# Optimization experiments

Hardware: AMD Instinct MI355X
Metric: run time of the kernel (lower is better)

Reference implementation:

```python
import jax, jax.numpy as jnp
import numpy as np

NA = 3        # anchors per scale
NC = 80       # classes
NO = NC + 5   # outputs per anchor
STRIDES = (8.0, 16.0, 32.0)


def setup_inputs() -> dict:
    key = jax.random.key(0)
    ks = jax.random.split(key, 10)
    inp = {
        "p0": jax.random.normal(ks[0], (16, 256, 80, 80), jnp.float32),
        "p1": jax.random.normal(ks[1], (16, 512, 40, 40), jnp.float32),
        "p2": jax.random.normal(ks[2], (16, 1024, 20, 20), jnp.float32),
        "w0": jax.random.normal(ks[3], (255, 256), jnp.float32) * 0.02,
        "b0": jax.random.normal(ks[4], (255,), jnp.float32) * 0.02,
        "w1": jax.random.normal(ks[5], (255, 512), jnp.float32) * 0.02,
        "b1": jax.random.normal(ks[6], (255,), jnp.float32) * 0.02,
        "w2": jax.random.normal(ks[7], (255, 1024), jnp.float32) * 0.02,
        "b2": jax.random.normal(ks[8], (255,), jnp.float32) * 0.02,
        # YOLOv5 default anchors (pixel units), shape [nl, na, 2]
        "anchors": jnp.asarray(np.array(
            [[[10, 13], [16, 30], [33, 23]],
             [[30, 61], [62, 45], [59, 119]],
             [[116, 90], [156, 198], [373, 326]]], dtype=np.float32)),
    }
    return inp


def _decode_scale(p, w, b, anc, stride):
    # p: [bs, C, ny, nx]; w: [na*no, C]; anc: [na, 2] pixel anchors
    bs, _, ny, nx = p.shape
    y = jnp.einsum('bchw,oc->bohw', p, w) + b[None, :, None, None]   # 1x1 conv
    y = y.reshape(bs, NA, NO, ny, nx).transpose(0, 1, 3, 4, 2)       # [bs,na,ny,nx,no]
    s = jax.nn.sigmoid(y)
    gy, gx = jnp.meshgrid(jnp.arange(ny, dtype=p.dtype),
                          jnp.arange(nx, dtype=p.dtype), indexing='ij')
    grid = jnp.stack((gx, gy), axis=-1)[None, None] - 0.5            # [1,1,ny,nx,2]
    xy = (s[..., :2] * 2 + grid) * stride
    wh = (s[..., 2:4] * 2) ** 2 * anc.reshape(1, NA, 1, 1, 2)
    out = jnp.concatenate((xy, wh, s[..., 4:]), axis=-1)
    return out.reshape(bs, NA * ny * nx, NO)


def reference(p0, p1, p2, w0, b0, w1, b1, w2, b2, anchors):
    feats = (p0, p1, p2)
    ws = (w0, w1, w2)
    bs_ = (b0, b1, b2)
    z = [_decode_scale(feats[i], ws[i], bs_[i], anchors[i], STRIDES[i])
         for i in range(3)]
    return jnp.concatenate(z, axis=1)  # [bs, sum(na*ny*nx), no]
```

## Files before the change

kernel.cpp:

```cpp
#include <hip/hip_runtime.h>
#include <math.h>


#define NOUT 85
#define TOTAL_ROWS 25200

typedef __attribute__((ext_vector_type(8))) short short8;
typedef __attribute__((ext_vector_type(4))) float floatx4;

__device__ __forceinline__ unsigned short f2bf(float x) {
    union { float f; unsigned u; } v; v.f = x;
    unsigned r = v.u + 0x7fffu + ((v.u >> 16) & 1u);
    return (unsigned short)(r >> 16);
}

__global__ __launch_bounds__(256) void convert_w_all(
    const float* __restrict__ w0, const float* __restrict__ w1,
    const float* __restrict__ w2, unsigned short* __restrict__ dst)
{
    int i = blockIdx.x * 256 + threadIdx.x;
    const float* w; int C, idx;
    if (i < 65536)       { w = w0; C = 256;  idx = i; }
    else if (i < 196608) { w = w1; C = 512;  idx = i - 65536; }
    else                 { w = w2; C = 1024; idx = i - 196608; }
    int j  = idx & 7;
    int l  = (idx >> 3) & 63;
    int t  = idx >> 9;
    int ot = t & 15, kt = t >> 4;
    int o  = ot * 16 + (l & 15);
    int k  = kt * 32 + (l >> 4) * 8 + j;
    float v = (o < 255) ? w[(size_t)o * C + k] : 0.f;
    dst[i] = f2bf(v);
}

__global__ __launch_bounds__(256) void yolo_fused(
    const float* __restrict__ p0, const float* __restrict__ p1,
    const float* __restrict__ p2, const unsigned short* __restrict__ wsA,
    const float* __restrict__ b0v, const float* __restrict__ b1v,
    const float* __restrict__ b2v, const float* __restrict__ anc,
    float* __restrict__ out)
{
    __shared__ __align__(16) unsigned short Bl0[64 * 32];
    __shared__ __align__(16) unsigned short Bl1[64 * 32];

    const int tid = threadIdx.x;
    const int l   = tid & 63;
    const int wv  = tid >> 6;
    const int ml  = l & 15;
    const int q   = l >> 4;

    const int x = blockIdx.x;
    const float* p; const unsigned short* wA; const float* bias; const float* an;
    int C, HW, row_off, sh, tile, b; float stride_;
    if (x < 112) {
        b = x / 7;  tile = x - b * 7;
        p = p2; wA = wsA + 196608; bias = b2v; an = anc + 12;
        C = 1024; HW = 400; row_off = 24000; sh = 2; stride_ = 32.f;
    } else if (x < 512) {
        int i = x - 112; b = i / 25; tile = i - b * 25;
        p = p1; wA = wsA + 65536; bias = b1v; an = anc + 6;
        C = 512; HW = 1600; row_off = 19200; sh = 3; stride_ = 16.f;
    } else {
        int i = x - 512; b = i / 100; tile = i - b * 100;
        p = p0; wA = wsA; bias = b0v; an = anc;
        C = 256; HW = 6400; row_off = 0; sh = 4; stride_ = 8.f;
    }
    const int hw0   = tile * 64;
    const int iters = C >> 5;

    floatx4 acc[4][4];
#pragma unroll
    for (int ni = 0; ni < 4; ++ni)
#pragma unroll
        for (int mi = 0; mi < 4; ++mi)
            acc[ni][mi] = floatx4{0.f, 0.f, 0.f, 0.f};

    const float* pb = p + (size_t)b * C * HW;
    int scol = hw0 + l; if (scol >= HW) scol = HW - 1;
    const float* pcol0 = pb + (size_t)(wv * 8) * HW + scol;
    const size_t kj = (size_t)32 * HW;

    const int wchunk = wv ^ (l & 3) ^ ((l >> 2) & 3);
    const unsigned short* wfb = wA + ((size_t)(wv * 4) << 9) + (l << 3);

    float  bvA[8], bvB[8];
    short8 wfA[4], wfB[4];

#define LOADBV(dst, s) do { const float* _pc = pcol0 + (size_t)(s) * kj;          \
        _Pragma("unroll") for (int _r = 0; _r < 8; ++_r)                          \
            dst[_r] = _pc[(size_t)_r * HW]; } while (0)
#define LOADWF(dst, s) do { const unsigned short* _wb = wfb + (size_t)(s) * 8192; \
        _Pragma("unroll") for (int _m = 0; _m < 4; ++_m)                          \
            dst[_m] = *(const short8*)(_wb + (_m << 9)); } while (0)
#define PACK(src, BUF) do {                                                       \
        unsigned _p0 = (unsigned)f2bf(src[0]) | ((unsigned)f2bf(src[1]) << 16);   \
        unsigned _p1 = (unsigned)f2bf(src[2]) | ((unsigned)f2bf(src[3]) << 16);   \
        unsigned _p2 = (unsigned)f2bf(src[4]) | ((unsigned)f2bf(src[5]) << 16);   \
        unsigned _p3 = (unsigned)f2bf(src[6]) | ((unsigned)f2bf(src[7]) << 16);   \
        ((uint4*)BUF)[l * 4 + wchunk] = make_uint4(_p0, _p1, _p2, _p3); } while (0)
#define READPF(pf, BUF) do { _Pragma("unroll") for (int _n = 0; _n < 4; ++_n) {   \
        int _nn = _n * 16 + ml; int _ck = q ^ (_nn & 3) ^ ((_nn >> 2) & 3);       \
        pf[_n] = *(const short8*)(BUF + _nn * 32 + _ck * 8); } } while (0)
#define MFMA16(pf, wf) do { _Pragma("unroll") for (int _n = 0; _n < 4; ++_n)      \
        _Pragma("unroll") for (int _m = 0; _m < 4; ++_m)                          \
            acc[_n][_m] = __builtin_amdgcn_mfma_f32_16x16x32_bf16(                \
                pf[_n], wf[_m], acc[_n][_m], 0, 0, 0); } while (0)
#define LGKM_BARRIER() do { asm volatile("s_waitcnt lgkmcnt(0)" ::: "memory");    \
        __builtin_amdgcn_s_barrier(); asm volatile("" ::: "memory"); } while (0)

    LOADBV(bvA, 0);
    LOADBV(bvB, 1);
    LOADWF(wfA, 0);
    PACK(bvA, Bl0);
    LOADBV(bvA, 2);
    LGKM_BARRIER();

    for (int it = 0; it < iters; it += 2) {
        short8 pfA[4];
        READPF(pfA, Bl0);
        PACK(bvB, Bl1);
        if (it + 3 < iters) LOADBV(bvB, it + 3);
        LOADWF(wfB, it + 1);
        LGKM_BARRIER();
        MFMA16(pfA, wfA);

        short8 pfB[4];
        READPF(pfB, Bl1);
        if (it + 2 < iters) {
            PACK(bvA, Bl0);
            if (it + 4 < iters) LOADBV(bvA, it + 4);
            LOADWF(wfA, it + 2);
            LGKM_BARRIER();
        }
        MFMA16(pfB, wfB);
    }

    const int nx = 5 << sh;
#pragma unroll
    for (int mi = 0; mi < 4; ++mi) {
        const int  o     = wv * 64 + mi * 16 + ml;
        const bool valid = (o < 255);
        const int  osafe = valid ? o : 254;
        const int  a     = osafe / 85;
        const int  oo    = osafe - a * 85;
        const float bi   = bias[osafe];
        const float anw  = an[a * 2 + 0];
        const float anh  = an[a * 2 + 1];
        float* orow = out + ((size_t)b * TOTAL_ROWS + row_off + a * HW) * NOUT + oo;
#pragma unroll
        for (int ni = 0; ni < 4; ++ni) {
            const int hwb = hw0 + ni * 16 + q * 4;
            if (hwb >= HW) continue;
#pragma unroll
            for (int r = 0; r < 4; ++r) {
                const int hw = hwb + r;
                float y = acc[ni][mi][r] + bi;
                float s = 1.f / (1.f + __expf(-y));
                float v;
                if (oo >= 4) {
                    v = s;
                } else {
                    unsigned gy = (unsigned)(((unsigned long long)(unsigned)(hw >> sh)
                                             * 0xCCCCCCCDull) >> 34);
                    int gx = hw - (int)gy * nx;
                    if (oo == 0)      v = (2.f * s + (float)gx - 0.5f) * stride_;
                    else if (oo == 1) v = (2.f * s + (float)gy - 0.5f) * stride_;
                    else { float t = 2.f * s; v = t * t * ((oo == 2) ? anw : anh); }
                }
                if (valid) orow[(size_t)hw * NOUT] = v;
            }
        }
    }
#undef LOADBV
#undef LOADWF
#undef PACK
#undef READPF
#undef MFMA16
#undef LGKM_BARRIER
}

extern "C" void kernel_launch(void* const* d_in, const int* in_sizes, int n_in,
                              void* d_out, int out_size, void* d_ws, size_t ws_size,
                              hipStream_t stream) {
    const float* p0 = (const float*)d_in[0];
    const float* p1 = (const float*)d_in[1];
    const float* p2 = (const float*)d_in[2];
    const float* w0 = (const float*)d_in[3];
    const float* b0 = (const float*)d_in[4];
    const float* w1 = (const float*)d_in[5];
    const float* b1 = (const float*)d_in[6];
    const float* w2 = (const float*)d_in[7];
    const float* b2 = (const float*)d_in[8];
    const float* anc = (const float*)d_in[9];
    float* out = (float*)d_out;

    unsigned short* wsA = (unsigned short*)d_ws;

    convert_w_all<<<dim3(458752 / 256), dim3(256), 0, stream>>>(w0, w1, w2, wsA);

    yolo_fused<<<dim3(2112), dim3(256), 0, stream>>>(
        p0, p1, p2, wsA, b0, b1, b2, anc, out);
}
```

Measured before the change: 339.9 us.

## Pre-convert activations to bf16 MFMA fragment layout in separate pass

Adds a pre-pass kernel that converts all three feature maps to bf16 and writes them to workspace in the exact MFMA fragment order. A new GEMM kernel then loads activation and weight fragments straight from global memory into registers, with no LDS staging and no barriers, double-buffering the loads. This removes the per-block packing and synchronisation, at the cost of an extra full read of the fp32 inputs plus a bf16 write and re-read. The new path runs only when the workspace is large enough, and otherwise falls back to the fused kernel.

New measurement: 374.7 us. 1.1x slower.

```diff
diff --git a/kernel.cpp b/kernel.cpp
--- a/kernel.cpp
+++ b/kernel.cpp
@@ -4,6 +4,18 @@
 
 #define NOUT 85
 #define TOTAL_ROWS 25200
+
+#define WOFF0 0
+#define WOFF1 65536
+#define WOFF2 196608
+#define PFRAG_OFF 458752
+#define PSZ0 26214400
+#define PSZ1 13107200
+#define PSZ2 7340032
+#define POFF0 (PFRAG_OFF)
+#define POFF1 (PFRAG_OFF + PSZ0)
+#define POFF2 (PFRAG_OFF + PSZ0 + PSZ1)
+#define WS_NEED_FULL ((size_t)(PFRAG_OFF + PSZ0 + PSZ1 + PSZ2) * 2)
 
 typedef __attribute__((ext_vector_type(8))) short short8;
 typedef __attribute__((ext_vector_type(4))) float floatx4;
@@ -33,6 +45,147 @@
     dst[i] = f2bf(v);
 }
 
+__global__ __launch_bounds__(256) void convert_p_all(
+    const float* __restrict__ p0, const float* __restrict__ p1,
+    const float* __restrict__ p2, unsigned short* __restrict__ ws)
+{
+    int i = blockIdx.x * 256 + threadIdx.x;
+    const float* p; int C, HW; int b, t, s, lc;
+    if (i < 3276800) {
+        p = p0; C = 256; HW = 6400;
+        lc = i & 255; s = (i >> 8) & 7;  int bt = i >> 11;
+        b = bt / 100; t = bt - b * 100;
+    } else if (i < 4915200) {
+        int idx = i - 3276800;
+        p = p1; C = 512; HW = 1600;
+        lc = idx & 255; s = (idx >> 8) & 15; int bt = idx >> 12;
+        b = bt / 25;  t = bt - b * 25;
+    } else {
+        int idx = i - 4915200;
+        p = p2; C = 1024; HW = 400;
+        lc = idx & 255; s = (idx >> 8) & 31; int bt = idx >> 13;
+        b = bt / 7;   t = bt - b * 7;
+    }
+    int ni = lc >> 6, l = lc & 63, q = l >> 4, ml = l & 15;
+    int hw = t * 64 + ni * 16 + ml; if (hw >= HW) hw = HW - 1;
+    const float* src = p + ((size_t)b * C + (s * 32 + q * 8)) * HW + hw;
+    unsigned d[4];
+#pragma unroll
+    for (int r = 0; r < 4; ++r) {
+        float a  = src[(size_t)(2 * r) * HW];
+        float bb = src[(size_t)(2 * r + 1) * HW];
+        d[r] = (unsigned)f2bf(a) | ((unsigned)f2bf(bb) << 16);
+    }
+    ((uint4*)(ws + PFRAG_OFF))[(size_t)i] = make_uint4(d[0], d[1], d[2], d[3]);
+}
+
+__global__ __launch_bounds__(256) void yolo_gemm(
+    const unsigned short* __restrict__ ws,
+    const float* __restrict__ b0v, const float* __restrict__ b1v,
+    const float* __restrict__ b2v, const float* __restrict__ anc,
+    float* __restrict__ out)
+{
+    const int tid = threadIdx.x;
+    const int l   = tid & 63;
+    const int wv  = tid >> 6;
+    const int ml  = l & 15;
+    const int q   = l >> 4;
+
+    const int x = blockIdx.x;
+    const float* bias; const float* an;
+    int C, HW, row_off, sh, tile, b, T; size_t wOff, pOff; float stride_;
+    if (x < 112) {
+        b = x / 7;  tile = x - b * 7;  T = 7;
+        wOff = WOFF2; pOff = POFF2; bias = b2v; an = anc + 12;
+        C = 1024; HW = 400; row_off = 24000; sh = 2; stride_ = 32.f;
+    } else if (x < 512) {
+        int i = x - 112; b = i / 25; tile = i - b * 25; T = 25;
+        wOff = WOFF1; pOff = POFF1; bias = b1v; an = anc + 6;
+        C = 512; HW = 1600; row_off = 19200; sh = 3; stride_ = 16.f;
+    } else {
+        int i = x - 512; b = i / 100; tile = i - b * 100; T = 100;
+        wOff = WOFF0; pOff = POFF0; bias = b0v; an = anc;
+        C = 256; HW = 6400; row_off = 0; sh = 4; stride_ = 8.f;
+    }
+    const int hw0 = tile * 64;
+    const int S   = C >> 5;
+
+    const unsigned short* pfp = ws + pOff + (size_t)(b * T + tile) * S * 2048 + (l << 3);
+    const unsigned short* wfp = ws + wOff + ((size_t)(wv * 4) << 9) + (l << 3);
+
+    floatx4 acc[4][4];
+#pragma unroll
+    for (int ni = 0; ni < 4; ++ni)
+#pragma unroll
+        for (int mi = 0; mi < 4; ++mi)
+            acc[ni][mi] = floatx4{0.f, 0.f, 0.f, 0.f};
+
+#define GLOADP(dst, s_) do { const unsigned short* _b = pfp + (size_t)(s_) * 2048;  \
+        _Pragma("unroll") for (int _n = 0; _n < 4; ++_n)                            \
+            dst[_n] = *(const short8*)(_b + (_n << 9)); } while (0)
+#define GLOADW(dst, s_) do { const unsigned short* _b = wfp + (size_t)(s_) * 8192;  \
+        _Pragma("unroll") for (int _m = 0; _m < 4; ++_m)                            \
+            dst[_m] = *(const short8*)(_b + (_m << 9)); } while (0)
+#define GMFMA(pf, wf) do { _Pragma("unroll") for (int _n = 0; _n < 4; ++_n)         \
+        _Pragma("unroll") for (int _m = 0; _m < 4; ++_m)                            \
+            acc[_n][_m] = __builtin_amdgcn_mfma_f32_16x16x32_bf16(                  \
+                pf[_n], wf[_m], acc[_n][_m], 0, 0, 0); } while (0)
+
+    short8 pfA[4], wfA[4], pfB[4], wfB[4];
+    GLOADP(pfA, 0); GLOADW(wfA, 0);
+    GLOADP(pfB, 1); GLOADW(wfB, 1);
+
+    int s = 0;
+    for (; s + 2 < S; s += 2) {
+        GMFMA(pfA, wfA);
+        GLOADP(pfA, s + 2); GLOADW(wfA, s + 2);
+        GMFMA(pfB, wfB);
+        GLOADP(pfB, s + 3); GLOADW(wfB, s + 3);
+    }
+    GMFMA(pfA, wfA);
+    GMFMA(pfB, wfB);
+#undef GLOADP
+#undef GLOADW
+#undef GMFMA
+
+    const int nx = 5 << sh;
+#pragma unroll
+    for (int mi = 0; mi < 4; ++mi) {
+        const int  o     = wv * 64 + mi * 16 + ml;
+        const bool valid = (o < 255);
+        const int  osafe = valid ? o : 254;
+        const int  a     = osafe / 85;
+        const int  oo    = osafe - a * 85;
+        const float bi   = bias[osafe];
+        const float anw  = an[a * 2 + 0];
+        const float anh  = an[a * 2 + 1];
+        float* orow = out + ((size_t)b * TOTAL_ROWS + row_off + a * HW) * NOUT + oo;
+#pragma unroll
+        for (int ni = 0; ni < 4; ++ni) {
+            const int hwb = hw0 + ni * 16 + q * 4;
+            if (hwb >= HW) continue;
+#pragma unroll
+            for (int r = 0; r < 4; ++r) {
+                const int hw = hwb + r;
+                float y = acc[ni][mi][r] + bi;
+                float sg = 1.f / (1.f + __expf(-y));
+                float v;
+                if (oo >= 4) {
+                    v = sg;
+                } else {
+                    unsigned gy = (unsigned)(((unsigned long long)(unsigned)(hw >> sh)
+                                             * 0xCCCCCCCDull) >> 34);
+                    int gx = hw - (int)gy * nx;
+                    if (oo == 0)      v = (2.f * sg + (float)gx - 0.5f) * stride_;
+                    else if (oo == 1) v = (2.f * sg + (float)gy - 0.5f) * stride_;
+                    else { float tt = 2.f * sg; v = tt * tt * ((oo == 2) ? anw : anh); }
+                }
+                if (valid) orow[(size_t)hw * NOUT] = v;
+            }
+        }
+    }
+}
+
 __global__ __launch_bounds__(256) void yolo_fused(
     const float* __restrict__ p0, const float* __restrict__ p1,
     const float* __restrict__ p2, const unsigned short* __restrict__ wsA,
@@ -54,15 +207,15 @@
     int C, HW, row_off, sh, tile, b; float stride_;
     if (x < 112) {
         b = x / 7;  tile = x - b * 7;
-        p = p2; wA = wsA + 196608; bias = b2v; an = anc + 12;
+        p = p2; wA = wsA + WOFF2; bias = b2v; an = anc + 12;
         C = 1024; HW = 400; row_off = 24000; sh = 2; stride_ = 32.f;
     } else if (x < 512) {
         int i = x - 112; b = i / 25; tile = i - b * 25;
-        p = p1; wA = wsA + 65536; bias = b1v; an = anc + 6;
+        p = p1; wA = wsA + WOFF1; bias = b1v; an = anc + 6;
         C = 512; HW = 1600; row_off = 19200; sh = 3; stride_ = 16.f;
     } else {
         int i = x - 512; b = i / 100; tile = i - b * 100;
-        p = p0; wA = wsA; bias = b0v; an = anc;
+        p = p0; wA = wsA + WOFF0; bias = b0v; an = anc;
         C = 256; HW = 6400; row_off = 0; sh = 4; stride_ = 8.f;
     }
     const int hw0   = tile * 64;
@@ -155,17 +308,17 @@
             for (int r = 0; r < 4; ++r) {
                 const int hw = hwb + r;
                 float y = acc[ni][mi][r] + bi;
-                float s = 1.f / (1.f + __expf(-y));
+                float sg = 1.f / (1.f + __expf(-y));
                 float v;
                 if (oo >= 4) {
-                    v = s;
+                    v = sg;
                 } else {
                     unsigned gy = (unsigned)(((unsigned long long)(unsigned)(hw >> sh)
                                              * 0xCCCCCCCDull) >> 34);
                     int gx = hw - (int)gy * nx;
-                    if (oo == 0)      v = (2.f * s + (float)gx - 0.5f) * stride_;
-                    else if (oo == 1) v = (2.f * s + (float)gy - 0.5f) * stride_;
-                    else { float t = 2.f * s; v = t * t * ((oo == 2) ? anw : anh); }
+                    if (oo == 0)      v = (2.f * sg + (float)gx - 0.5f) * stride_;
+                    else if (oo == 1) v = (2.f * sg + (float)gy - 0.5f) * stride_;
+                    else { float tt = 2.f * sg; v = tt * tt * ((oo == 2) ? anw : anh); }
                 }
                 if (valid) orow[(size_t)hw * NOUT] = v;
             }
@@ -198,6 +351,12 @@
 
     convert_w_all<<<dim3(458752 / 256), dim3(256), 0, stream>>>(w0, w1, w2, wsA);
 
-    yolo_fused<<<dim3(2112), dim3(256), 0, stream>>>(
-        p0, p1, p2, wsA, b0, b1, b2, anc, out);
-}
+    if (ws_size >= WS_NEED_FULL) {
+        convert_p_all<<<dim3(22784), dim3(256), 0, stream>>>(p0, p1, p2, wsA);
+        yolo_gemm<<<dim3(2112), dim3(256), 0, stream>>>(
+            wsA, b0, b1, b2, anc, out);
+    } else {
+        yolo_fused<<<dim3(2112), dim3(256), 0, stream>>>(
+            p0, p1, p2, wsA, b0, b1, b2, anc, out);
+    }
+}
```

## Stage activation chunks in shared memory and coalesce output via LDS staging

Applied to the files above, without the earlier changes.

Replaces the per-iteration double-buffered activation pipeline with bulk chunked loads: each chunk of up to 512 channels is read as float4 vectors, converted to bf16 and stored into a swizzled 64KB shared buffer, then the MFMA loop runs over it. The epilogue writes results into shared memory and then copies them to global memory contiguously, instead of doing scattered stores with an 85-float stride. This targets uncoalesced loads and stores, but the 64KB LDS lowers occupancy and drops the overlap of loads with compute inside each chunk.

New measurement: 330.7 us. 2.7% less time.

```diff
diff --git a/kernel.cpp b/kernel.cpp
--- a/kernel.cpp
+++ b/kernel.cpp
@@ -4,6 +4,10 @@
 
 #define NOUT 85
 #define TOTAL_ROWS 25200
+
+#define WOFF0 0
+#define WOFF1 65536
+#define WOFF2 196608
 
 typedef __attribute__((ext_vector_type(8))) short short8;
 typedef __attribute__((ext_vector_type(4))) float floatx4;
@@ -33,15 +37,16 @@
     dst[i] = f2bf(v);
 }
 
-__global__ __launch_bounds__(256) void yolo_fused(
+__global__ __launch_bounds__(256) void yolo_fused2(
     const float* __restrict__ p0, const float* __restrict__ p1,
     const float* __restrict__ p2, const unsigned short* __restrict__ wsA,
     const float* __restrict__ b0v, const float* __restrict__ b1v,
     const float* __restrict__ b2v, const float* __restrict__ anc,
     float* __restrict__ out)
 {
-    __shared__ __align__(16) unsigned short Bl0[64 * 32];
-    __shared__ __align__(16) unsigned short Bl1[64 * 32];
+    __shared__ __align__(16) unsigned char smem[65536];
+    unsigned short* act = (unsigned short*)smem;
+    float*          ob  = (float*)smem;
 
     const int tid = threadIdx.x;
     const int l   = tid & 63;
@@ -54,19 +59,21 @@
     int C, HW, row_off, sh, tile, b; float stride_;
     if (x < 112) {
         b = x / 7;  tile = x - b * 7;
-        p = p2; wA = wsA + 196608; bias = b2v; an = anc + 12;
+        p = p2; wA = wsA + WOFF2; bias = b2v; an = anc + 12;
         C = 1024; HW = 400; row_off = 24000; sh = 2; stride_ = 32.f;
     } else if (x < 512) {
         int i = x - 112; b = i / 25; tile = i - b * 25;
-        p = p1; wA = wsA + 65536; bias = b1v; an = anc + 6;
+        p = p1; wA = wsA + WOFF1; bias = b1v; an = anc + 6;
         C = 512; HW = 1600; row_off = 19200; sh = 3; stride_ = 16.f;
     } else {
         int i = x - 512; b = i / 100; tile = i - b * 100;
-        p = p0; wA = wsA; bias = b0v; an = anc;
+        p = p0; wA = wsA + WOFF0; bias = b0v; an = anc;
         C = 256; HW = 6400; row_off = 0; sh = 4; stride_ = 8.f;
     }
-    const int hw0   = tile * 64;
-    const int iters = C >> 5;
+    const int hw0 = tile * 64;
+    const int S   = C >> 5;
+    const int Sc  = (S < 16) ? S : 16;
+    const int nch = (S > 16) ? (S >> 4) : 1;
 
     floatx4 acc[4][4];
 #pragma unroll
@@ -75,66 +82,71 @@
         for (int mi = 0; mi < 4; ++mi)
             acc[ni][mi] = floatx4{0.f, 0.f, 0.f, 0.f};
 
+    const int s_loc = tid >> 6;
+    const int co    = (tid >> 4) & 3;
+    const int hq    = tid & 15;
+    int hwq = hw0 + hq * 4;
+    if (hwq + 4 > HW) hwq = HW - 4;
     const float* pb = p + (size_t)b * C * HW;
-    int scol = hw0 + l; if (scol >= HW) scol = HW - 1;
-    const float* pcol0 = pb + (size_t)(wv * 8) * HW + scol;
-    const size_t kj = (size_t)32 * HW;
-
-    const int wchunk = wv ^ (l & 3) ^ ((l >> 2) & 3);
-    const unsigned short* wfb = wA + ((size_t)(wv * 4) << 9) + (l << 3);
-
-    float  bvA[8], bvB[8];
-    short8 wfA[4], wfB[4];
-
-#define LOADBV(dst, s) do { const float* _pc = pcol0 + (size_t)(s) * kj;          \
-        _Pragma("unroll") for (int _r = 0; _r < 8; ++_r)                          \
-            dst[_r] = _pc[(size_t)_r * HW]; } while (0)
-#define LOADWF(dst, s) do { const unsigned short* _wb = wfb + (size_t)(s) * 8192; \
-        _Pragma("unroll") for (int _m = 0; _m < 4; ++_m)                          \
-            dst[_m] = *(const short8*)(_wb + (_m << 9)); } while (0)
-#define PACK(src, BUF) do {                                                       \
-        unsigned _p0 = (unsigned)f2bf(src[0]) | ((unsigned)f2bf(src[1]) << 16);   \
-        unsigned _p1 = (unsigned)f2bf(src[2]) | ((unsigned)f2bf(src[3]) << 16);   \
-        unsigned _p2 = (unsigned)f2bf(src[4]) | ((unsigned)f2bf(src[5]) << 16);   \
-        unsigned _p3 = (unsigned)f2bf(src[6]) | ((unsigned)f2bf(src[7]) << 16);   \
-        ((uint4*)BUF)[l * 4 + wchunk] = make_uint4(_p0, _p1, _p2, _p3); } while (0)
-#define READPF(pf, BUF) do { _Pragma("unroll") for (int _n = 0; _n < 4; ++_n) {   \
-        int _nn = _n * 16 + ml; int _ck = q ^ (_nn & 3) ^ ((_nn >> 2) & 3);       \
-        pf[_n] = *(const short8*)(BUF + _nn * 32 + _ck * 8); } } while (0)
-#define MFMA16(pf, wf) do { _Pragma("unroll") for (int _n = 0; _n < 4; ++_n)      \
-        _Pragma("unroll") for (int _m = 0; _m < 4; ++_m)                          \
-            acc[_n][_m] = __builtin_amdgcn_mfma_f32_16x16x32_bf16(                \
+
+    const unsigned short* wfp = wA + ((size_t)(wv * 4) << 9) + (l << 3);
+
+#define LOADWF(dst, s_) do { const unsigned short* _b = wfp + (size_t)(s_) * 8192;  \
+        _Pragma("unroll") for (int _m = 0; _m < 4; ++_m)                            \
+            dst[_m] = *(const short8*)(_b + (_m << 9)); } while (0)
+#define READPF(pf, s_) do { _Pragma("unroll") for (int _n = 0; _n < 4; ++_n) {      \
+        int _a16 = (((s_) * 4 + _n) << 6) + l; _a16 ^= (_a16 >> 4) & 7;             \
+        pf[_n] = *(const short8*)(act + (_a16 << 3)); } } while (0)
+#define GMFMA(pf, wf) do { _Pragma("unroll") for (int _n = 0; _n < 4; ++_n)         \
+        _Pragma("unroll") for (int _m = 0; _m < 4; ++_m)                            \
+            acc[_n][_m] = __builtin_amdgcn_mfma_f32_16x16x32_bf16(                  \
                 pf[_n], wf[_m], acc[_n][_m], 0, 0, 0); } while (0)
-#define LGKM_BARRIER() do { asm volatile("s_waitcnt lgkmcnt(0)" ::: "memory");    \
-        __builtin_amdgcn_s_barrier(); asm volatile("" ::: "memory"); } while (0)
-
-    LOADBV(bvA, 0);
-    LOADBV(bvB, 1);
-    LOADWF(wfA, 0);
-    PACK(bvA, Bl0);
-    LOADBV(bvA, 2);
-    LGKM_BARRIER();
-
-    for (int it = 0; it < iters; it += 2) {
-        short8 pfA[4];
-        READPF(pfA, Bl0);
-        PACK(bvB, Bl1);
-        if (it + 3 < iters) LOADBV(bvB, it + 3);
-        LOADWF(wfB, it + 1);
-        LGKM_BARRIER();
-        MFMA16(pfA, wfA);
-
-        short8 pfB[4];
-        READPF(pfB, Bl1);
-        if (it + 2 < iters) {
-            PACK(bvA, Bl0);
-            if (it + 4 < iters) LOADBV(bvA, it + 4);
-            LOADWF(wfA, it + 2);
-            LGKM_BARRIER();
+
+    for (int ch = 0; ch < nch; ++ch) {
+        if (ch) __syncthreads();
+        const int cb = ch * Sc * 32;
+
+        for (int r = 0; r < (Sc >> 2); ++r) {
+            const int s = r * 4 + s_loc;
+            const int c = cb + s * 32 + co * 8;
+            floatx4 v[8];
+#pragma unroll
+            for (int i = 0; i < 8; ++i)
+                v[i] = *(const floatx4*)(pb + (size_t)(c + i) * HW + hwq);
+#pragma unroll
+            for (int e = 0; e < 4; ++e) {
+                const int hwr = hq * 4 + e;
+                const int ni = hwr >> 4, mll = hwr & 15;
+                unsigned d0 = (unsigned)f2bf(v[0][e]) | ((unsigned)f2bf(v[1][e]) << 16);
+                unsigned d1 = (unsigned)f2bf(v[2][e]) | ((unsigned)f2bf(v[3][e]) << 16);
+                unsigned d2 = (unsigned)f2bf(v[4][e]) | ((unsigned)f2bf(v[5][e]) << 16);
+                unsigned d3 = (unsigned)f2bf(v[6][e]) | ((unsigned)f2bf(v[7][e]) << 16);
+                int a16 = ((s * 4 + ni) << 6) + co * 16 + mll;
+                a16 ^= (a16 >> 4) & 7;
+                *(uint4*)(act + (a16 << 3)) = make_uint4(d0, d1, d2, d3);
+            }
         }
-        MFMA16(pfB, wfB);
-    }
-
+        __syncthreads();
+
+        const int gs0 = ch * Sc;
+        short8 wfA[4], wfB[4];
+        LOADWF(wfA, gs0);
+        LOADWF(wfB, gs0 + 1);
+        for (int s = 0; s < Sc; s += 2) {
+            short8 pfA[4], pfB[4];
+            READPF(pfA, s);
+            GMFMA(pfA, wfA);
+            if (s + 2 < Sc) LOADWF(wfA, gs0 + s + 2);
+            READPF(pfB, s + 1);
+            GMFMA(pfB, wfB);
+            if (s + 3 < Sc) LOADWF(wfB, gs0 + s + 3);
+        }
+    }
+#undef LOADWF
+#undef READPF
+#undef GMFMA
+
+    __syncthreads();
     const int nx = 5 << sh;
 #pragma unroll
     for (int mi = 0; mi < 4; ++mi) {
@@ -146,37 +158,44 @@
         const float bi   = bias[osafe];
         const float anw  = an[a * 2 + 0];
         const float anh  = an[a * 2 + 1];
-        float* orow = out + ((size_t)b * TOTAL_ROWS + row_off + a * HW) * NOUT + oo;
+        const int  lbase = a * 5440 + oo;
 #pragma unroll
         for (int ni = 0; ni < 4; ++ni) {
-            const int hwb = hw0 + ni * 16 + q * 4;
-            if (hwb >= HW) continue;
-#pragma unroll
-            for (int r = 0; r < 4; ++r) {
-                const int hw = hwb + r;
-                float y = acc[ni][mi][r] + bi;
-                float s = 1.f / (1.f + __expf(-y));
+            const int hwr0 = ni * 16 + q * 4;
+            if (hw0 + hwr0 >= HW) continue;
+#pragma unroll
+            for (int rr = 0; rr < 4; ++rr) {
+                const int hwr = hwr0 + rr;
+                const int hw  = hw0 + hwr;
+                float y  = acc[ni][mi][rr] + bi;
+                float sg = 1.f / (1.f + __expf(-y));
                 float v;
                 if (oo >= 4) {
-                    v = s;
+                    v = sg;
                 } else {
                     unsigned gy = (unsigned)(((unsigned long long)(unsigned)(hw >> sh)
                                              * 0xCCCCCCCDull) >> 34);
                     int gx = hw - (int)gy * nx;
-                    if (oo == 0)      v = (2.f * s + (float)gx - 0.5f) * stride_;
-                    else if (oo == 1) v = (2.f * s + (float)gy - 0.5f) * stride_;
-                    else { float t = 2.f * s; v = t * t * ((oo == 2) ? anw : anh); }
+                    if (oo == 0)      v = (2.f * sg + (float)gx - 0.5f) * stride_;
+                    else if (oo == 1) v = (2.f * sg + (float)gy - 0.5f) * stride_;
+                    else { float tt = 2.f * sg; v = tt * tt * ((oo == 2) ? anw : anh); }
                 }
-                if (valid) orow[(size_t)hw * NOUT] = v;
+                if (valid) ob[lbase + hwr * 85] = v;
             }
         }
     }
-#undef LOADBV
-#undef LOADWF
-#undef PACK
-#undef READPF
-#undef MFMA16
-#undef LGKM_BARRIER
+    __syncthreads();
+
+    const int ne   = (HW - hw0 < 64) ? (HW - hw0) : 64;
+    const int ne85 = ne * 85;
+    float* gb = out + ((size_t)b * TOTAL_ROWS + row_off + hw0) * NOUT;
+    const size_t astr = (size_t)HW * NOUT;
+    const int ftot = 3 * ne85;
+    for (int f = tid; f < ftot; f += 256) {
+        int a  = (f >= ne85) + (f >= 2 * ne85);
+        int k2 = f - a * ne85;
+        gb[(size_t)a * astr + k2] = ob[a * 5440 + k2];
+    }
 }
 
 extern "C" void kernel_launch(void* const* d_in, const int* in_sizes, int n_in,
@@ -198,6 +217,6 @@
 
     convert_w_all<<<dim3(458752 / 256), dim3(256), 0, stream>>>(w0, w1, w2, wsA);
 
-    yolo_fused<<<dim3(2112), dim3(256), 0, stream>>>(
+    yolo_fused2<<<dim3(2112), dim3(256), 0, stream>>>(
         p0, p1, p2, wsA, b0, b1, b2, anc, out);
 }
```
